# Kernel tuning notes

Measured on AMD Instinct MI355X. Metric: run time of the kernel, lower is better.

Reference implementation:

```python
import jax, jax.numpy as jnp
import numpy as np

B, T, H = 16, 64, 256  # batch, timesteps (= num stacked layers), hidden
L = T                  # MultiRNNCell([cell]*timesteps): layers == timesteps, shared weights


def setup_inputs() -> dict:
    key = jax.random.key(0)
    k1, k2, k3 = jax.random.split(key, 3)
    x = jax.random.normal(k1, (B, T, H), dtype=jnp.float32)
    init_state = jax.random.normal(k2, (L, 2, B, H), dtype=jnp.float32) * 0.1  # [L, (c,h), B, H]
    W = jax.random.normal(k3, (2 * H, 4 * H), dtype=jnp.float32) / np.sqrt(2 * H)
    b = jnp.zeros((4 * H,), dtype=jnp.float32)
    return {"x": x, "init_state": init_state, "W": W, "b": b}


def reference(x, init_state, W, b):
    # TF LSTMCell math: gates order (i, j, f, o), forget_bias = 1.0
    c0 = init_state[:, 0]  # [L,B,H]
    h0 = init_state[:, 1]  # [L,B,H]

    def layer_fn(inp, st):
        # inp: [B,H] input to this layer; st = (c,h) each [B,H]
        lc, lh = st
        z = jnp.concatenate([inp, lh], axis=-1) @ W + b  # [B,4H]
        i, j, f, o = jnp.split(z, 4, axis=-1)
        nc = jax.nn.sigmoid(f + 1.0) * lc + jax.nn.sigmoid(i) * jnp.tanh(j)
        nh = jax.nn.sigmoid(o) * jnp.tanh(nc)
        return nh, (nc, nh)  # carry = input to next layer; ys = new per-layer state

    def step(carry, xt):
        # carry: (c,h) each [L,B,H]; xt: [B,H]
        c, h = carry
        top_h, (nc, nh) = jax.lax.scan(layer_fn, xt, (c, h))
        return (nc, nh), top_h

    (_, _), ys = jax.lax.scan(step, (c0, h0), jnp.transpose(x, (1, 0, 2)))  # ys: [T,B,H]
    return jnp.transpose(ys, (1, 0, 2))  # [B,T,H] top-layer outputs (dynamic_rnn outputs)
```

## Files before the change

kernel.cpp:

```cpp
#include <hip/hip_runtime.h>

typedef _Float16 half8 __attribute__((ext_vector_type(8)));
typedef float f32x4 __attribute__((ext_vector_type(4)));
typedef unsigned int u32;
typedef unsigned int u32x4 __attribute__((ext_vector_type(4)));

#define SC_AGENT __HIP_MEMORY_SCOPE_AGENT

constexpr size_t OFF_PROG  = 0;
constexpr size_t OFF_EPOCH = 4096;
constexpr size_t OFF_H     = 65536;
constexpr size_t S4 = (size_t)64 * 16 * 256;

__device__ __forceinline__ float sigm(float v) { return 1.0f / (1.0f + __expf(-v)); }
__device__ __forceinline__ float tanh_(float v) { return 1.0f - 2.0f / (__expf(2.0f * v) + 1.0f); }
__device__ __forceinline__ u32 min4(u32x4 v) {
  u32 a = v[0] < v[1] ? v[0] : v[1];
  u32 b = v[2] < v[3] ? v[2] : v[3];
  return a < b ? a : b;
}

#define GLD4(dst, base, OFS)                                                  \
  asm volatile("global_load_dwordx4 %0, %1, off offset:" #OFS " sc0 sc1"      \
               : "=v"(dst) : "v"(base))

__global__ void bump_epoch(char* ws) {
  u32* ep = (u32*)(ws + OFF_EPOCH);
  u32 v = __hip_atomic_load(ep, __ATOMIC_RELAXED, SC_AGENT);
  u32 n = (v + 1) & 0x1FFu;
  if (n == 0) n = 1;
  __hip_atomic_store(ep, n, __ATOMIC_RELAXED, SC_AGENT);
}

__global__ void init_ws(const float* __restrict__ init_state, char* ws) {
  u32* prog = (u32*)(ws + OFF_PROG);
  u32* Hw4 = (u32*)(ws + OFF_H);
  const u32 ep = __hip_atomic_load((u32*)(ws + OFF_EPOCH), __ATOMIC_RELAXED, SC_AGENT);
  const u32 epb = (ep & 0x1FFu) << 7;
  const int tid = blockIdx.x * 256 + threadIdx.x;
  if (tid < 256) prog[tid] = epb - 1u;
  const u32 tagInit = (epb | 127u) << 16;
  for (int e = tid; e < 64 * 16 * 256; e += 65536) {
    const int u = e & 255, b = (e >> 8) & 15, l = e >> 12;
    const size_t idx = ((size_t)l * 16 + b) * 256 + u;
    Hw4[idx] = 0u;
    union { _Float16 f; unsigned short s; } hv;
    hv.f = (_Float16)init_state[((l * 2 + 1) * 16 + b) * 256 + u];
    Hw4[S4 + idx] = (u32)hv.s | tagInit;
  }
}

__global__ __launch_bounds__(256, 1) void lstm_mfma(
    const float* __restrict__ x, const float* __restrict__ init_state,
    const float* __restrict__ W, const float* __restrict__ bias,
    float* __restrict__ out, char* ws) {
  u32* prog = (u32*)(ws + OFF_PROG);
  u32* Hw4 = (u32*)(ws + OFF_H);

  const int tid = threadIdx.x;
  const int wg = blockIdx.x;
  const int l = wg >> 2, r = wg & 3;
  const int wv = tid >> 6, lane = tid & 63;

  const u32 epb = (__hip_atomic_load((u32*)(ws + OFF_EPOCH), __ATOMIC_RELAXED,
                                     SC_AGENT) & 0x1FFu) << 7;

  __shared__ alignas(16) _Float16 aLds[16 * 64 * 8];

  half8 wreg[64];
#pragma unroll
  for (int q = 0; q < 4; ++q) {
    const int nl = (wv * 4 + q) * 16 + (lane & 15);
    const int col = (nl & 3) * 256 + r * 64 + (nl >> 2);
#pragma unroll
    for (int kb = 0; kb < 16; ++kb) {
      const int k0 = kb * 32 + (lane >> 4) * 8;
      const float* src = W + (size_t)k0 * 1024 + col;
      half8 hv;
#pragma unroll
      for (int jj = 0; jj < 8; ++jj) hv[jj] = (_Float16)src[(size_t)jj * 1024];
      wreg[q * 16 + kb] = hv;
    }
  }

  const int m_own = (lane >> 4) * 4 + (lane & 3);
  int gu_q[4];
  float creg[4], bI[4], bJ[4], bF[4], bO[4];
#pragma unroll
  for (int q = 0; q < 4; ++q) {
    const int u_q = (wv * 4 + q) * 4 + ((lane & 15) >> 2);
    gu_q[q] = r * 64 + u_q;
    creg[q] = init_state[((l * 2 + 0) * 16 + m_own) * 256 + gu_q[q]];
    bI[q] = bias[0 * 256 + gu_q[q]];
    bJ[q] = bias[1 * 256 + gu_q[q]];
    bF[q] = bias[2 * 256 + gu_q[q]];
    bO[q] = bias[3 * 256 + gu_q[q]];
  }

#pragma unroll
  for (int q = 0; q < 4; ++q) {
    const int gu = gu_q[q];
    const float h0 = init_state[((l * 2 + 1) * 16 + m_own) * 256 + gu];
    aLds[(size_t)((8 + (gu >> 5)) * 64 + ((((gu & 31) >> 3) << 4) | m_own)) * 8 +
         (gu & 7)] = (_Float16)h0;
  }

  const int m = lane & 15;
  const int ksub = (lane >> 4) * 8;
  const u32 ownMask = ((wv >> 1) == r) ? 0x30u
                    : (((wv + 4) >> 1) == r) ? 0xC0u : 0u;

  u32 plCache = 0, bpCache = 0;
  u32* const plBase = &prog[(l > 0 ? l - 1 : 0) * 4];
  u32* const bpBase = &prog[(l < 63 ? l + 1 : 63) * 4];

  for (int t = 0; t < 64; ++t) {
    const int slotCur = t & 1, slotPrev = (t + 1) & 1;
    const u32 expIn = epb | (u32)t;
    const u32 expOwn = (t > 0) ? (epb | (u32)(t - 1)) : (epb | 127u);

    if (l == 0) {
#pragma unroll
      for (int i = 0; i < 2; ++i) {
        const int kb = i * 4 + wv;
        const int k0 = kb * 32 + ksub;
        const float* xs = x + ((size_t)m * 64 + t) * 256 + k0;
        half8 hv;
#pragma unroll
        for (int jj = 0; jj < 8; ++jj) hv[jj] = (_Float16)xs[jj];
        *(half8*)&aLds[(size_t)(kb * 64 + lane) * 8] = hv;
      }
    }

    unsigned pend = ((l == 0) ? 0xF0u : 0xFFu) & ~ownMask;
    const bool bpNeed = (tid == 0 && l < 63 && t >= 2);
    bool bpOK = !bpNeed || bpCache >= (epb | (u32)(t - 2));
    const u32* pLow = Hw4 + (slotCur ? S4 : 0) +
                      (((size_t)(l > 0 ? l - 1 : 0) * 16 + m) * 256) + wv * 32 + ksub;
    const u32* pHigh = Hw4 + (slotPrev ? S4 : 0) +
                       (((size_t)l * 16 + m) * 256) + wv * 32 + ksub;
    int round = 0;
    while (pend || !bpOK) {
      const bool ready = (l == 0) || (plCache >= (epb | (u32)t));
      const bool didData = ready && pend;
      u32x4 gv[8], pv, bv;
      if (didData) {
        if (pend & 0x01u) GLD4(gv[0], pLow, 0);
        if (pend & 0x02u) GLD4(gv[1], pLow, 16);
        if (pend & 0x04u) GLD4(gv[2], pLow, 512);
        if (pend & 0x08u) GLD4(gv[3], pLow, 528);
        if (pend & 0x10u) GLD4(gv[4], pHigh, 0);
        if (pend & 0x20u) GLD4(gv[5], pHigh, 16);
        if (pend & 0x40u) GLD4(gv[6], pHigh, 512);
        if (pend & 0x80u) GLD4(gv[7], pHigh, 528);
      }
      const bool didGate = (l > 0) && !ready;
      if (didGate) GLD4(pv, plBase, 0);
      if (!bpOK) GLD4(bv, bpBase, 0);
      asm volatile("s_waitcnt vmcnt(0)" ::: "memory");
      __builtin_amdgcn_sched_barrier(0);
      if (didGate) plCache = min4(pv);
      if (!bpOK) {
        bpCache = min4(bv);
        bpOK = bpCache >= (epb | (u32)(t - 2));
      }
      if (didData) {
#pragma unroll
        for (int b = 0; b < 8; ++b) {
          if ((pend >> b) & 1u) {
            const u32 exp_ = (b < 4) ? expIn : expOwn;
            const u32x4 v = gv[b];
            if ((v[0] >> 16) == exp_ && (v[1] >> 16) == exp_ &&
                (v[2] >> 16) == exp_ && (v[3] >> 16) == exp_) {
              const int kb = (b >> 1) * 4 + wv;
              u32* dp = (u32*)&aLds[(size_t)(kb * 64 + lane) * 8 + (b & 1) * 4];
              dp[0] = (v[0] & 0xFFFFu) | (v[1] << 16);
              dp[1] = (v[2] & 0xFFFFu) | (v[3] << 16);
              pend &= ~(1u << b);
            }
          }
        }
      }
      if (pend || !bpOK) {
        if (++round > 500000) break;
        if (!ready) __builtin_amdgcn_s_sleep(4);
        else if (round > 64 && (round & 3) == 0) __builtin_amdgcn_s_sleep(1);
      }
    }
    __syncthreads();
    if (tid == 0)
      __hip_atomic_store(&prog[l * 4 + r], epb | (u32)t, __ATOMIC_RELAXED, SC_AGENT);

    f32x4 acc[4] = {{0.f, 0.f, 0.f, 0.f}, {0.f, 0.f, 0.f, 0.f},
                    {0.f, 0.f, 0.f, 0.f}, {0.f, 0.f, 0.f, 0.f}};
#pragma unroll
    for (int kb = 0; kb < 16; ++kb) {
      half8 a = *(const half8*)&aLds[(kb * 64 + lane) * 8];
#pragma unroll
      for (int q = 0; q < 4; ++q)
        acc[q] = __builtin_amdgcn_mfma_f32_16x16x32_f16(a, wreg[q * 16 + kb], acc[q], 0, 0, 0);
    }
    __syncthreads();

#pragma unroll
    for (int q = 0; q < 4; ++q) {
      float v0 = acc[q][0], v1 = acc[q][1], v2 = acc[q][2], v3 = acc[q][3];
      float e0 = __shfl_xor(v1, 1, 64), e1 = __shfl_xor(v0, 1, 64);
      float e2 = __shfl_xor(v3, 1, 64), e3 = __shfl_xor(v2, 1, 64);
      const bool o1 = (lane & 1);
      float m0 = o1 ? e0 : v0, m1 = o1 ? v1 : e1;
      float m2 = o1 ? e2 : v2, m3 = o1 ? v3 : e3;
      float f0 = __shfl_xor(m2, 2, 64), f1 = __shfl_xor(m3, 2, 64);
      float f2 = __shfl_xor(m0, 2, 64), f3 = __shfl_xor(m1, 2, 64);
      const bool o2 = (lane & 2);
      float gI = o2 ? f0 : m0, gJ = o2 ? f1 : m1;
      float gF = o2 ? m2 : f2, gO = o2 ? m3 : f3;

      const float iv = gI + bI[q], jv = gJ + bJ[q];
      const float fv = gF + bF[q], ov = gO + bO[q];
      const float nc = sigm(fv + 1.0f) * creg[q] + sigm(iv) * tanh_(jv);
      const float nh = sigm(ov) * tanh_(nc);
      creg[q] = nc;
      union { _Float16 f; unsigned short s; } cv;
      cv.f = (_Float16)nh;
      const int gu = gu_q[q];
      const size_t idx = (slotCur ? S4 : 0) +
                         ((size_t)l * 16 + m_own) * 256 + gu;
      __hip_atomic_store(Hw4 + idx, (u32)cv.s | (expIn << 16),
                         __ATOMIC_RELAXED, SC_AGENT);
      aLds[(size_t)((8 + (gu >> 5)) * 64 + ((((gu & 31) >> 3) << 4) | m_own)) * 8 +
           (gu & 7)] = cv.f;
      if (l == 63) out[((size_t)m_own * 64 + t) * 256 + gu] = nh;
    }
  }
}

extern "C" void kernel_launch(void* const* d_in, const int* in_sizes, int n_in,
                              void* d_out, int out_size, void* d_ws,
                              size_t ws_size, hipStream_t stream) {
  const float* x          = (const float*)d_in[0];
  const float* init_state = (const float*)d_in[1];
  const float* W          = (const float*)d_in[2];
  const float* bias       = (const float*)d_in[3];
  float* out = (float*)d_out;
  char* ws   = (char*)d_ws;

  bump_epoch<<<1, 1, 0, stream>>>(ws);
  init_ws<<<256, 256, 0, stream>>>(init_state, ws);
  lstm_mfma<<<256, 256, 0, stream>>>(x, init_state, W, bias, out, ws);
}
```

Before: 686.0 us.

## Stage h outputs in LDS and publish with coalesced 16-byte stores

Each block now writes its new h values into a small LDS staging buffer and, after a barrier, publishes them to the global exchange buffer with one 16-byte store per thread. This replaces scattered 4-byte atomic stores. The consumer-side read mapping is reworked to match: each lane reads 4 contiguous units per row, the own-slice mask changes, and LDS placement goes through a precomputed index. The intent is fewer and wider global transactions on the inter-layer critical path, at the cost of an extra __syncthreads per timestep.

New measurement: 682.3 us. No clear change (-0.6%).

```diff
diff --git a/kernel.cpp b/kernel.cpp
--- a/kernel.cpp
+++ b/kernel.cpp
@@ -66,6 +66,7 @@
                                      SC_AGENT) & 0x1FFu) << 7;
 
   __shared__ alignas(16) _Float16 aLds[16 * 64 * 8];
+  __shared__ unsigned short hLds[16 * 68];
 
   half8 wreg[64];
 #pragma unroll
@@ -84,35 +85,37 @@
   }
 
   const int m_own = (lane >> 4) * 4 + (lane & 3);
-  int gu_q[4];
+  int uo_q[4];
   float creg[4], bI[4], bJ[4], bF[4], bO[4];
 #pragma unroll
   for (int q = 0; q < 4; ++q) {
-    const int u_q = (wv * 4 + q) * 4 + ((lane & 15) >> 2);
-    gu_q[q] = r * 64 + u_q;
-    creg[q] = init_state[((l * 2 + 0) * 16 + m_own) * 256 + gu_q[q]];
-    bI[q] = bias[0 * 256 + gu_q[q]];
-    bJ[q] = bias[1 * 256 + gu_q[q]];
-    bF[q] = bias[2 * 256 + gu_q[q]];
-    bO[q] = bias[3 * 256 + gu_q[q]];
+    uo_q[q] = (wv * 4 + q) * 4 + ((lane & 15) >> 2);
+    const int gu = r * 64 + uo_q[q];
+    creg[q] = init_state[((l * 2 + 0) * 16 + m_own) * 256 + gu];
+    bI[q] = bias[0 * 256 + gu];
+    bJ[q] = bias[1 * 256 + gu];
+    bF[q] = bias[2 * 256 + gu];
+    bO[q] = bias[3 * 256 + gu];
   }
 
 #pragma unroll
   for (int q = 0; q < 4; ++q) {
-    const int gu = gu_q[q];
+    const int gu = r * 64 + uo_q[q];
     const float h0 = init_state[((l * 2 + 1) * 16 + m_own) * 256 + gu];
-    aLds[(size_t)((8 + (gu >> 5)) * 64 + ((((gu & 31) >> 3) << 4) | m_own)) * 8 +
+    aLds[(size_t)((8 + (gu >> 5)) * 64 + (((gu & 31) >> 3) << 4) + m_own) * 8 +
          (gu & 7)] = (_Float16)h0;
   }
 
-  const int m = lane & 15;
-  const int ksub = (lane >> 4) * 8;
-  const u32 ownMask = ((wv >> 1) == r) ? 0x30u
-                    : (((wv + 4) >> 1) == r) ? 0xC0u : 0u;
+  const int u0 = lane * 4;
+  const int idxB = (u0 >> 5) * 512 + (((u0 & 31) >> 3) * 16 + wv) * 8 + (u0 & 7);
+  const u32 ownMask = ((lane >> 4) == r) ? 0xF0u : 0u;
 
   u32 plCache = 0, bpCache = 0;
   u32* const plBase = &prog[(l > 0 ? l - 1 : 0) * 4];
   u32* const bpBase = &prog[(l < 63 ? l + 1 : 63) * 4];
+
+  const int m = lane & 15;
+  const int ksub = (lane >> 4) * 8;
 
   for (int t = 0; t < 64; ++t) {
     const int slotCur = t & 1, slotPrev = (t + 1) & 1;
@@ -135,24 +138,25 @@
     unsigned pend = ((l == 0) ? 0xF0u : 0xFFu) & ~ownMask;
     const bool bpNeed = (tid == 0 && l < 63 && t >= 2);
     bool bpOK = !bpNeed || bpCache >= (epb | (u32)(t - 2));
-    const u32* pLow = Hw4 + (slotCur ? S4 : 0) +
-                      (((size_t)(l > 0 ? l - 1 : 0) * 16 + m) * 256) + wv * 32 + ksub;
-    const u32* pHigh = Hw4 + (slotPrev ? S4 : 0) +
-                       (((size_t)l * 16 + m) * 256) + wv * 32 + ksub;
+    const u32* pLa = Hw4 + (slotCur ? S4 : 0) +
+                     ((size_t)(l > 0 ? l - 1 : 0) << 12) + wv * 256 + u0 + 1024;
+    const u32* pLb = pLa + 2048;
+    const u32* pHa = Hw4 + (slotPrev ? S4 : 0) + ((size_t)l << 12) + wv * 256 + u0 + 1024;
+    const u32* pHb = pHa + 2048;
     int round = 0;
     while (pend || !bpOK) {
       const bool ready = (l == 0) || (plCache >= (epb | (u32)t));
       const bool didData = ready && pend;
       u32x4 gv[8], pv, bv;
       if (didData) {
-        if (pend & 0x01u) GLD4(gv[0], pLow, 0);
-        if (pend & 0x02u) GLD4(gv[1], pLow, 16);
-        if (pend & 0x04u) GLD4(gv[2], pLow, 512);
-        if (pend & 0x08u) GLD4(gv[3], pLow, 528);
-        if (pend & 0x10u) GLD4(gv[4], pHigh, 0);
-        if (pend & 0x20u) GLD4(gv[5], pHigh, 16);
-        if (pend & 0x40u) GLD4(gv[6], pHigh, 512);
-        if (pend & 0x80u) GLD4(gv[7], pHigh, 528);
+        if (pend & 0x01u) GLD4(gv[0], pLa, -4096);
+        if (pend & 0x02u) GLD4(gv[1], pLa, 0);
+        if (pend & 0x04u) GLD4(gv[2], pLb, -4096);
+        if (pend & 0x08u) GLD4(gv[3], pLb, 0);
+        if (pend & 0x10u) GLD4(gv[4], pHa, -4096);
+        if (pend & 0x20u) GLD4(gv[5], pHa, 0);
+        if (pend & 0x40u) GLD4(gv[6], pHb, -4096);
+        if (pend & 0x80u) GLD4(gv[7], pHb, 0);
       }
       const bool didGate = (l > 0) && !ready;
       if (didGate) GLD4(pv, plBase, 0);
@@ -166,17 +170,17 @@
       }
       if (didData) {
 #pragma unroll
-        for (int b = 0; b < 8; ++b) {
-          if ((pend >> b) & 1u) {
-            const u32 exp_ = (b < 4) ? expIn : expOwn;
-            const u32x4 v = gv[b];
+        for (int bit = 0; bit < 8; ++bit) {
+          if ((pend >> bit) & 1u) {
+            const u32 exp_ = (bit < 4) ? expIn : expOwn;
+            const u32x4 v = gv[bit];
             if ((v[0] >> 16) == exp_ && (v[1] >> 16) == exp_ &&
                 (v[2] >> 16) == exp_ && (v[3] >> 16) == exp_) {
-              const int kb = (b >> 1) * 4 + wv;
-              u32* dp = (u32*)&aLds[(size_t)(kb * 64 + lane) * 8 + (b & 1) * 4];
+              const int hf = bit >> 2, s = bit & 3;
+              u32* dp = (u32*)&aLds[idxB + hf * 4096 + s * 32];
               dp[0] = (v[0] & 0xFFFFu) | (v[1] << 16);
               dp[1] = (v[2] & 0xFFFFu) | (v[3] << 16);
-              pend &= ~(1u << b);
+              pend &= ~(1u << bit);
             }
           }
         }
@@ -223,14 +227,23 @@
       creg[q] = nc;
       union { _Float16 f; unsigned short s; } cv;
       cv.f = (_Float16)nh;
-      const int gu = gu_q[q];
-      const size_t idx = (slotCur ? S4 : 0) +
-                         ((size_t)l * 16 + m_own) * 256 + gu;
-      __hip_atomic_store(Hw4 + idx, (u32)cv.s | (expIn << 16),
-                         __ATOMIC_RELAXED, SC_AGENT);
-      aLds[(size_t)((8 + (gu >> 5)) * 64 + ((((gu & 31) >> 3) << 4) | m_own)) * 8 +
+      const int gu = r * 64 + uo_q[q];
+      aLds[(size_t)((8 + (gu >> 5)) * 64 + (((gu & 31) >> 3) << 4) + m_own) * 8 +
            (gu & 7)] = cv.f;
+      hLds[m_own * 68 + uo_q[q]] = cv.s;
       if (l == 63) out[((size_t)m_own * 64 + t) * 256 + gu] = nh;
+    }
+    __syncthreads();
+
+    {
+      const int sb = tid >> 4, so0 = (tid & 15) * 4;
+      u32x4 pub;
+#pragma unroll
+      for (int j = 0; j < 4; ++j)
+        pub[j] = (u32)hLds[sb * 68 + so0 + j] | (expIn << 16);
+      u32* dst = Hw4 + (slotCur ? S4 : 0) + ((size_t)l << 12) + sb * 256 + r * 64 + so0;
+      asm volatile("global_store_dwordx4 %0, %1, off sc0 sc1"
+                   :: "v"(dst), "v"(pub) : "memory");
     }
   }
 }
```
